# Kernel tuning notes

Measured on AMD Instinct MI355X. Metric: run time of the kernel, lower is better.

The kernel has to match this reference:

```python
import jax, jax.numpy as jnp
import numpy as np

S = 8192  # sequence length
D = 256   # feature dim


def setup_inputs() -> dict:
    key = jax.random.key(0)
    kq, kk, kv = jax.random.split(key, 3)
    Q = jax.random.normal(kq, (S, D), dtype=jnp.float32)
    K = jax.random.normal(kk, (S, D), dtype=jnp.float32)
    V = jax.random.normal(kv, (S, D), dtype=jnp.float32)
    return {"Q": Q, "K": K, "V": V}


def reference(Q, K, V):
    # Faithful to the torch module: dk = K.size(-2) (the SEQUENCE length, not head dim)
    dk = K.shape[-2]
    scores = (Q @ K.T) / jnp.sqrt(jnp.float32(dk))  # [S, S]
    # F.softmax with implicit dim on a 2D tensor -> softmax over last dim (keys)
    attn = jax.nn.softmax(scores, axis=-1)
    return attn @ V  # [S, D]
```

## Files before the change

kernel.cpp:

```cpp
#include <hip/hip_runtime.h>


typedef __attribute__((ext_vector_type(4))) float    f32x4;
typedef __attribute__((ext_vector_type(8))) short    s16x8;
typedef __attribute__((ext_vector_type(4))) int      i32x4;
typedef __attribute__((ext_vector_type(4))) _Float16 f16x4;
typedef int  __attribute__((may_alias)) int_a;
typedef long __attribute__((may_alias)) long_a;

#define SEQ 8192
#define DIM 256
#define NSPLIT 8
#define KPS (SEQ / NSPLIT)
#define BN 32
#define ITERS (KPS / BN)
#define BM 128

#define KSC (1.4426950408889634f / 90.50966799187808f)

static __device__ inline short f2bf(float f) {
    unsigned u = __float_as_uint(f);
    return (short)((u + 0x7FFFu + ((u >> 16) & 1u)) >> 16);
}
static __device__ inline short f2bf_fast(float f) {
    return (short)((__float_as_uint(f) + 0x8000u) >> 16);
}

__global__ void __launch_bounds__(256)
prep(const float* __restrict__ Q, const float* __restrict__ K,
     const float* __restrict__ V, unsigned char* __restrict__ Q8,
     unsigned char* __restrict__ K8, short* __restrict__ Vt) {
    __shared__ short tile[32][264];
    int b = blockIdx.x, t = threadIdx.x;

    {
        int row = b * 32 + (t >> 3);
        int c0 = (t & 7) * 8;
        const f32x4* q4 = (const f32x4*)Q + (size_t)row * 64 + c0;
        const f32x4* k4 = (const f32x4*)K + (size_t)row * 64 + c0;
        int qo[8], ko[8];
        #pragma unroll
        for (int i = 0; i < 8; ++i) {
            f32x4 q = q4[i], k = k4[i];
            int dq = 0, dk = 0;
            dq = __builtin_amdgcn_cvt_pk_fp8_f32(q.x, q.y, dq, false);
            dq = __builtin_amdgcn_cvt_pk_fp8_f32(q.z, q.w, dq, true);
            dk = __builtin_amdgcn_cvt_pk_fp8_f32(k.x, k.y, dk, false);
            dk = __builtin_amdgcn_cvt_pk_fp8_f32(k.z, k.w, dk, true);
            qo[i] = dq; ko[i] = dk;
        }
        i32x4* qd = (i32x4*)(Q8 + (size_t)row * 256 + (t & 7) * 32);
        i32x4* kd = (i32x4*)(K8 + (size_t)row * 256 + (t & 7) * 32);
        qd[0] = *(i32x4*)&qo[0]; qd[1] = *(i32x4*)&qo[4];
        kd[0] = *(i32x4*)&ko[0]; kd[1] = *(i32x4*)&ko[4];
    }

    #pragma unroll
    for (int i = 0; i < 8; ++i) {
        int c = t + i * 256;
        int row = c >> 6, col = c & 63;
        f32x4 v = ((const f32x4*)V)[(size_t)(b * 32 + row) * 64 + col];
        tile[row][col * 4 + 0] = f2bf(v.x);
        tile[row][col * 4 + 1] = f2bf(v.y);
        tile[row][col * 4 + 2] = f2bf(v.z);
        tile[row][col * 4 + 3] = f2bf(v.w);
    }
    __syncthreads();
    short* dst = Vt + (size_t)b * 8192 + t * 32;
    #pragma unroll
    for (int k8 = 0; k8 < 4; ++k8) {
        s16x8 w;
        #pragma unroll
        for (int j = 0; j < 8; ++j) w[j] = tile[k8 * 8 + j][t];
        *(s16x8*)(dst + k8 * 8) = w;
    }
}

__global__ void __launch_bounds__(256, 2)
attn(const unsigned char* __restrict__ Q8, const unsigned char* __restrict__ K8,
     const short* __restrict__ Vt, _Float16* __restrict__ Op,
     float* __restrict__ lp) {
    __shared__ unsigned char K_lds[32][272];
    __shared__ short V_lds[256][40];
    __shared__ short P_lds[4][32][34];

    int tid = threadIdx.x;
    int wid = tid >> 6, lane = tid & 63;
    int l15 = lane & 15, qq = lane >> 4;
    int qt = blockIdx.x >> 3, sp = blockIdx.x & 7;
    int qrow0 = qt * BM + wid * 32;

    long qf[2][8];
    #pragma unroll
    for (int t = 0; t < 2; ++t) {
        const unsigned char* p = Q8 + (size_t)(qrow0 + t * 16 + l15) * DIM + qq * 8;
        #pragma unroll
        for (int s = 0; s < 8; ++s) qf[t][s] = *(const long_a*)(p + s * 32);
    }

    s16x8 of;
    #pragma unroll
    for (int j = 0; j < 8; ++j) of[j] = (l15 == 0) ? (short)0x3F80 : (short)0;

    const unsigned char* ksrc = K8 + (size_t)(sp * KPS + (tid >> 4)) * DIM + (tid & 15) * 16;
    unsigned char* kdst = &K_lds[tid >> 4][(tid & 15) * 16];
    const short* vsrc = Vt + (size_t)sp * (KPS / BN) * 8192 + (tid >> 2) * 32 + (tid & 3) * 8;
    short* vdst = &V_lds[tid >> 2][(tid & 3) * 8];

    f32x4 acc[2][16] = {};
    f32x4 accl[2] = {};

    for (int it = 0; it < ITERS; ++it) {
        __syncthreads();
        *(i32x4*)kdst              = *(const i32x4*)ksrc;
        *(i32x4*)(kdst + 16 * 272) = *(const i32x4*)(ksrc + 16 * DIM);
        #pragma unroll
        for (int p = 0; p < 4; ++p)
            *(s16x8*)(vdst + p * 64 * 40) = *(const s16x8*)(vsrc + p * 64 * 32);
        ksrc += BN * DIM;
        vsrc += 8192;
        __syncthreads();

        f32x4 sc[2][2] = {};
        #pragma unroll
        for (int s = 0; s < 8; ++s) {
            long kf0 = *(const long_a*)&K_lds[l15][s * 32 + qq * 8];
            long kf1 = *(const long_a*)&K_lds[16 + l15][s * 32 + qq * 8];
            #pragma unroll
            for (int t = 0; t < 2; ++t) {
                sc[t][0] = __builtin_amdgcn_mfma_f32_16x16x32_fp8_fp8(qf[t][s], kf0, sc[t][0], 0, 0, 0);
                sc[t][1] = __builtin_amdgcn_mfma_f32_16x16x32_fp8_fp8(qf[t][s], kf1, sc[t][1], 0, 0, 0);
            }
        }

        #pragma unroll
        for (int t = 0; t < 2; ++t)
            #pragma unroll
            for (int r = 0; r < 4; ++r) {
                float e0 = fminf(sc[t][0][r] * KSC, 16.0f);
                float e1 = fminf(sc[t][1][r] * KSC, 16.0f);
                P_lds[wid][t * 16 + qq * 4 + r][l15]      = f2bf_fast(__builtin_amdgcn_exp2f(e0));
                P_lds[wid][t * 16 + qq * 4 + r][16 + l15] = f2bf_fast(__builtin_amdgcn_exp2f(e1));
            }
        const int_a* pb = (const int_a*)&P_lds[wid][0][0];
        union { int u[4]; s16x8 v; } p0, p1;
        #pragma unroll
        for (int w = 0; w < 4; ++w) {
            p0.u[w] = pb[l15 * 17 + qq * 4 + w];
            p1.u[w] = pb[(16 + l15) * 17 + qq * 4 + w];
        }

        #pragma unroll
        for (int n = 0; n < 16; ++n) {
            s16x8 vf = *(const s16x8*)&V_lds[n * 16 + l15][qq * 8];
            acc[0][n] = __builtin_amdgcn_mfma_f32_16x16x32_bf16(p0.v, vf, acc[0][n], 0, 0, 0);
            acc[1][n] = __builtin_amdgcn_mfma_f32_16x16x32_bf16(p1.v, vf, acc[1][n], 0, 0, 0);
        }
        accl[0] = __builtin_amdgcn_mfma_f32_16x16x32_bf16(p0.v, of, accl[0], 0, 0, 0);
        accl[1] = __builtin_amdgcn_mfma_f32_16x16x32_bf16(p1.v, of, accl[1], 0, 0, 0);
    }

    #pragma unroll
    for (int t = 0; t < 2; ++t) {
        #pragma unroll
        for (int n = 0; n < 16; ++n)
            #pragma unroll
            for (int r = 0; r < 4; ++r) {
                int row = qrow0 + t * 16 + qq * 4 + r;
                Op[((size_t)sp * SEQ + row) * DIM + n * 16 + l15] = (_Float16)acc[t][n][r];
            }
        if (l15 == 0) {
            #pragma unroll
            for (int r = 0; r < 4; ++r)
                lp[(size_t)sp * SEQ + qrow0 + t * 16 + qq * 4 + r] = accl[t][r];
        }
    }
}

__global__ void combine(const _Float16* __restrict__ Op, const float* __restrict__ lp,
                        float* __restrict__ out) {
    int idx = blockIdx.x * 256 + threadIdx.x;
    int row = idx >> 6;
    f32x4 a = {};
    float l = 0.0f;
    #pragma unroll
    for (int s = 0; s < NSPLIT; ++s) {
        f16x4 h = *(const f16x4*)(Op + (size_t)s * SEQ * DIM + (size_t)idx * 4);
        a.x += (float)h.x; a.y += (float)h.y; a.z += (float)h.z; a.w += (float)h.w;
        l += lp[s * SEQ + row];
    }
    float linv = 1.0f / (l + 1e-20f);
    ((f32x4*)out)[idx] = a * linv;
}

extern "C" void kernel_launch(void* const* d_in, const int* in_sizes, int n_in,
                              void* d_out, int out_size, void* d_ws, size_t ws_size,
                              hipStream_t stream) {
    const float* Q = (const float*)d_in[0];
    const float* K = (const float*)d_in[1];
    const float* V = (const float*)d_in[2];
    float* out = (float*)d_out;

    char* ws = (char*)d_ws;
    unsigned char* Q8 = (unsigned char*)ws;
    unsigned char* K8 = (unsigned char*)(ws + (2u << 20));
    short*    Vt = (short*)(ws + (4u << 20));
    _Float16* Op = (_Float16*)(ws + (8u << 20));
    float*    lp = (float*)(ws + (40u << 20));

    prep   <<<256, 256, 0, stream>>>(Q, K, V, Q8, K8, Vt);
    attn   <<<NSPLIT * (SEQ / BM), 256, 0, stream>>>(Q8, K8, Vt, Op, lp);
    combine<<<2048, 256, 0, stream>>>(Op, lp, out);
}
```

Measured before the change: 156.7 us.

## Double-buffer K/V tiles and keep P in registers via transposed score MFMA

Double-buffers the K and V shared-memory tiles. The next tile's global loads are issued into registers before the compute and written to the other buffer afterward, so each iteration needs one barrier instead of two. The score MFMA operands are swapped so the exp'd probabilities come out already in the fp16 A-operand layout of a 16x16x16 MFMA. This removes the per-wave P_lds round trip through shared memory, and V and P switch from bf16 to fp16. The cost is twice the MFMA instruction count at half K depth, extra registers for prefetch and doubled LDS, which may reduce occupancy.

```diff
diff --git a/kernel.cpp b/kernel.cpp
--- a/kernel.cpp
+++ b/kernel.cpp
@@ -2,11 +2,13 @@
 
 
 typedef __attribute__((ext_vector_type(4))) float    f32x4;
-typedef __attribute__((ext_vector_type(8))) short    s16x8;
 typedef __attribute__((ext_vector_type(4))) int      i32x4;
-typedef __attribute__((ext_vector_type(4))) _Float16 f16x4;
-typedef int  __attribute__((may_alias)) int_a;
+typedef __attribute__((ext_vector_type(4))) _Float16 h4;
+typedef __attribute__((ext_vector_type(8))) _Float16 h8;
 typedef long __attribute__((may_alias)) long_a;
+typedef i32x4 __attribute__((may_alias)) i32x4_a;
+typedef h4    __attribute__((may_alias)) h4_a;
+typedef h8    __attribute__((may_alias)) h8_a;
 
 #define SEQ 8192
 #define DIM 256
@@ -18,19 +20,11 @@
 
 #define KSC (1.4426950408889634f / 90.50966799187808f)
 
-static __device__ inline short f2bf(float f) {
-    unsigned u = __float_as_uint(f);
-    return (short)((u + 0x7FFFu + ((u >> 16) & 1u)) >> 16);
-}
-static __device__ inline short f2bf_fast(float f) {
-    return (short)((__float_as_uint(f) + 0x8000u) >> 16);
-}
-
 __global__ void __launch_bounds__(256)
 prep(const float* __restrict__ Q, const float* __restrict__ K,
      const float* __restrict__ V, unsigned char* __restrict__ Q8,
-     unsigned char* __restrict__ K8, short* __restrict__ Vt) {
-    __shared__ short tile[32][264];
+     unsigned char* __restrict__ K8, _Float16* __restrict__ Vt) {
+    __shared__ _Float16 tile[32][264];
     int b = blockIdx.x, t = threadIdx.x;
 
     {
@@ -60,35 +54,34 @@
         int c = t + i * 256;
         int row = c >> 6, col = c & 63;
         f32x4 v = ((const f32x4*)V)[(size_t)(b * 32 + row) * 64 + col];
-        tile[row][col * 4 + 0] = f2bf(v.x);
-        tile[row][col * 4 + 1] = f2bf(v.y);
-        tile[row][col * 4 + 2] = f2bf(v.z);
-        tile[row][col * 4 + 3] = f2bf(v.w);
+        tile[row][col * 4 + 0] = (_Float16)v.x;
+        tile[row][col * 4 + 1] = (_Float16)v.y;
+        tile[row][col * 4 + 2] = (_Float16)v.z;
+        tile[row][col * 4 + 3] = (_Float16)v.w;
     }
     __syncthreads();
-    short* dst = Vt + (size_t)b * 8192 + t * 32;
+    _Float16* dst = Vt + (size_t)b * 8192 + t * 32;
     #pragma unroll
     for (int k8 = 0; k8 < 4; ++k8) {
-        s16x8 w;
+        h8 w;
         #pragma unroll
         for (int j = 0; j < 8; ++j) w[j] = tile[k8 * 8 + j][t];
-        *(s16x8*)(dst + k8 * 8) = w;
+        *(h8*)(dst + k8 * 8) = w;
     }
 }
 
 __global__ void __launch_bounds__(256, 2)
 attn(const unsigned char* __restrict__ Q8, const unsigned char* __restrict__ K8,
-     const short* __restrict__ Vt, _Float16* __restrict__ Op,
+     const _Float16* __restrict__ Vt, _Float16* __restrict__ Op,
      float* __restrict__ lp) {
-    __shared__ unsigned char K_lds[32][272];
-    __shared__ short V_lds[256][40];
-    __shared__ short P_lds[4][32][34];
+    __shared__ unsigned char K_lds[2][32][272];
+    __shared__ _Float16 V_lds[2][256][40];
 
     int tid = threadIdx.x;
     int wid = tid >> 6, lane = tid & 63;
     int l15 = lane & 15, qq = lane >> 4;
-    int qt = blockIdx.x >> 3, sp = blockIdx.x & 7;
-    int qrow0 = qt * BM + wid * 32;
+    int qt_blk = blockIdx.x >> 3, sp = blockIdx.x & 7;
+    int qrow0 = qt_blk * BM + wid * 32;
 
     long qf[2][8];
     #pragma unroll
@@ -98,66 +91,85 @@
         for (int s = 0; s < 8; ++s) qf[t][s] = *(const long_a*)(p + s * 32);
     }
 
-    s16x8 of;
-    #pragma unroll
-    for (int j = 0; j < 8; ++j) of[j] = (l15 == 0) ? (short)0x3F80 : (short)0;
+    _Float16 one = (l15 == 0) ? (_Float16)1.0f : (_Float16)0.0f;
+    h4 of = {one, one, one, one};
 
     const unsigned char* ksrc = K8 + (size_t)(sp * KPS + (tid >> 4)) * DIM + (tid & 15) * 16;
-    unsigned char* kdst = &K_lds[tid >> 4][(tid & 15) * 16];
-    const short* vsrc = Vt + (size_t)sp * (KPS / BN) * 8192 + (tid >> 2) * 32 + (tid & 3) * 8;
-    short* vdst = &V_lds[tid >> 2][(tid & 3) * 8];
+    const _Float16* vsrc = Vt + (size_t)sp * (KPS / BN) * 8192 + (tid >> 2) * 32 + (tid & 3) * 8;
+    int kr = tid >> 4, kc = (tid & 15) * 16;
+    int vr = tid >> 2, vc = (tid & 3) * 8;
 
     f32x4 acc[2][16] = {};
     f32x4 accl[2] = {};
+    i32x4 kreg[2];
+    h8 vreg[4];
+
+    kreg[0] = *(const i32x4_a*)ksrc;
+    kreg[1] = *(const i32x4_a*)(ksrc + 16 * DIM);
+    #pragma unroll
+    for (int p = 0; p < 4; ++p) vreg[p] = *(const h8_a*)(vsrc + p * 64 * 32);
+    ksrc += BN * DIM; vsrc += 8192;
+    *(i32x4_a*)&K_lds[0][kr][kc]      = kreg[0];
+    *(i32x4_a*)&K_lds[0][kr + 16][kc] = kreg[1];
+    #pragma unroll
+    for (int p = 0; p < 4; ++p) *(h8_a*)&V_lds[0][vr + p * 64][vc] = vreg[p];
+    __syncthreads();
 
     for (int it = 0; it < ITERS; ++it) {
-        __syncthreads();
-        *(i32x4*)kdst              = *(const i32x4*)ksrc;
-        *(i32x4*)(kdst + 16 * 272) = *(const i32x4*)(ksrc + 16 * DIM);
-        #pragma unroll
-        for (int p = 0; p < 4; ++p)
-            *(s16x8*)(vdst + p * 64 * 40) = *(const s16x8*)(vsrc + p * 64 * 32);
-        ksrc += BN * DIM;
-        vsrc += 8192;
-        __syncthreads();
+        int b = it & 1;
+        if (it + 1 < ITERS) {
+            kreg[0] = *(const i32x4_a*)ksrc;
+            kreg[1] = *(const i32x4_a*)(ksrc + 16 * DIM);
+            #pragma unroll
+            for (int p = 0; p < 4; ++p) vreg[p] = *(const h8_a*)(vsrc + p * 64 * 32);
+            ksrc += BN * DIM; vsrc += 8192;
+        }
 
         f32x4 sc[2][2] = {};
         #pragma unroll
         for (int s = 0; s < 8; ++s) {
-            long kf0 = *(const long_a*)&K_lds[l15][s * 32 + qq * 8];
-            long kf1 = *(const long_a*)&K_lds[16 + l15][s * 32 + qq * 8];
+            long kf0 = *(const long_a*)&K_lds[b][l15][s * 32 + qq * 8];
+            long kf1 = *(const long_a*)&K_lds[b][16 + l15][s * 32 + qq * 8];
             #pragma unroll
             for (int t = 0; t < 2; ++t) {
-                sc[t][0] = __builtin_amdgcn_mfma_f32_16x16x32_fp8_fp8(qf[t][s], kf0, sc[t][0], 0, 0, 0);
-                sc[t][1] = __builtin_amdgcn_mfma_f32_16x16x32_fp8_fp8(qf[t][s], kf1, sc[t][1], 0, 0, 0);
+                sc[0][t] = __builtin_amdgcn_mfma_f32_16x16x32_fp8_fp8(kf0, qf[t][s], sc[0][t], 0, 0, 0);
+                sc[1][t] = __builtin_amdgcn_mfma_f32_16x16x32_fp8_fp8(kf1, qf[t][s], sc[1][t], 0, 0, 0);
             }
         }
 
-        #pragma unroll
-        for (int t = 0; t < 2; ++t)
-            #pragma unroll
-            for (int r = 0; r < 4; ++r) {
-                float e0 = fminf(sc[t][0][r] * KSC, 16.0f);
-                float e1 = fminf(sc[t][1][r] * KSC, 16.0f);
-                P_lds[wid][t * 16 + qq * 4 + r][l15]      = f2bf_fast(__builtin_amdgcn_exp2f(e0));
-                P_lds[wid][t * 16 + qq * 4 + r][16 + l15] = f2bf_fast(__builtin_amdgcn_exp2f(e1));
-            }
-        const int_a* pb = (const int_a*)&P_lds[wid][0][0];
-        union { int u[4]; s16x8 v; } p0, p1;
-        #pragma unroll
-        for (int w = 0; w < 4; ++w) {
-            p0.u[w] = pb[l15 * 17 + qq * 4 + w];
-            p1.u[w] = pb[(16 + l15) * 17 + qq * 4 + w];
-        }
+        h4 pfrag[2][2];
+        #pragma unroll
+        for (int kt = 0; kt < 2; ++kt)
+            #pragma unroll
+            for (int t = 0; t < 2; ++t)
+                #pragma unroll
+                for (int r = 0; r < 4; ++r) {
+                    float e = fminf(sc[kt][t][r] * KSC, 16.0f);
+                    pfrag[kt][t][r] = (_Float16)__builtin_amdgcn_exp2f(e);
+                }
 
         #pragma unroll
         for (int n = 0; n < 16; ++n) {
-            s16x8 vf = *(const s16x8*)&V_lds[n * 16 + l15][qq * 8];
-            acc[0][n] = __builtin_amdgcn_mfma_f32_16x16x32_bf16(p0.v, vf, acc[0][n], 0, 0, 0);
-            acc[1][n] = __builtin_amdgcn_mfma_f32_16x16x32_bf16(p1.v, vf, acc[1][n], 0, 0, 0);
-        }
-        accl[0] = __builtin_amdgcn_mfma_f32_16x16x32_bf16(p0.v, of, accl[0], 0, 0, 0);
-        accl[1] = __builtin_amdgcn_mfma_f32_16x16x32_bf16(p1.v, of, accl[1], 0, 0, 0);
+            h4 vf0 = *(const h4_a*)&V_lds[b][n * 16 + l15][qq * 4];
+            h4 vf1 = *(const h4_a*)&V_lds[b][n * 16 + l15][16 + qq * 4];
+            acc[0][n] = __builtin_amdgcn_mfma_f32_16x16x16f16(pfrag[0][0], vf0, acc[0][n], 0, 0, 0);
+            acc[0][n] = __builtin_amdgcn_mfma_f32_16x16x16f16(pfrag[1][0], vf1, acc[0][n], 0, 0, 0);
+            acc[1][n] = __builtin_amdgcn_mfma_f32_16x16x16f16(pfrag[0][1], vf0, acc[1][n], 0, 0, 0);
+            acc[1][n] = __builtin_amdgcn_mfma_f32_16x16x16f16(pfrag[1][1], vf1, acc[1][n], 0, 0, 0);
+        }
+        accl[0] = __builtin_amdgcn_mfma_f32_16x16x16f16(pfrag[0][0], of, accl[0], 0, 0, 0);
+        accl[0] = __builtin_amdgcn_mfma_f32_16x16x16f16(pfrag[1][0], of, accl[0], 0, 0, 0);
+        accl[1] = __builtin_amdgcn_mfma_f32_16x16x16f16(pfrag[0][1], of, accl[1], 0, 0, 0);
+        accl[1] = __builtin_amdgcn_mfma_f32_16x16x16f16(pfrag[1][1], of, accl[1], 0, 0, 0);
+
+        if (it + 1 < ITERS) {
+            int nb = b ^ 1;
+            *(i32x4_a*)&K_lds[nb][kr][kc]      = kreg[0];
+            *(i32x4_a*)&K_lds[nb][kr + 16][kc] = kreg[1];
+            #pragma unroll
+            for (int p = 0; p < 4; ++p) *(h8_a*)&V_lds[nb][vr + p * 64][vc] = vreg[p];
+            __syncthreads();
+        }
     }
 
     #pragma unroll
@@ -185,7 +197,7 @@
     float l = 0.0f;
     #pragma unroll
     for (int s = 0; s < NSPLIT; ++s) {
-        f16x4 h = *(const f16x4*)(Op + (size_t)s * SEQ * DIM + (size_t)idx * 4);
+        h4 h = *(const h4*)(Op + (size_t)s * SEQ * DIM + (size_t)idx * 4);
         a.x += (float)h.x; a.y += (float)h.y; a.z += (float)h.z; a.w += (float)h.w;
         l += lp[s * SEQ + row];
     }
@@ -204,7 +216,7 @@
     char* ws = (char*)d_ws;
     unsigned char* Q8 = (unsigned char*)ws;
     unsigned char* K8 = (unsigned char*)(ws + (2u << 20));
-    short*    Vt = (short*)(ws + (4u << 20));
+    _Float16* Vt = (_Float16*)(ws + (4u << 20));
     _Float16* Op = (_Float16*)(ws + (8u << 20));
     float*    lp = (float*)(ws + (40u << 20));
 
```

Result: slower. 160.3 us (+2.3%).
